# Kernel tuning notes

Measured on AMD Instinct MI355X. Metric: run time of the kernel, lower is better.

## Reference

```python
import jax, jax.numpy as jnp
import numpy as np

B, F0, D = 4096, 39, 16
CIN = [128, 128, 128]


def setup_inputs() -> dict:
    key = jax.random.key(0)
    ks = jax.random.split(key, 4)
    x = jax.random.normal(ks[0], (B, F0, D), dtype=jnp.float32)
    fields = [F0] + CIN
    inp = {"embedded_features": x}
    for i in range(len(CIN)):
        cin = F0 * fields[i]
        cout = fields[i + 1]
        kw = jax.random.fold_in(ks[1], i)
        # Conv1d default init scale ~ 1/sqrt(fan_in)
        inp[f"W{i}"] = jax.random.normal(kw, (cout, cin), dtype=jnp.float32) / np.sqrt(cin)
        inp[f"b{i}"] = jnp.zeros((cout,), dtype=jnp.float32)
    return inp


def _cin_layer(X0, Xi, W, b):
    # Math identical to: outer_product [B,F0,Fi,D] -> reshape [B,F0*Fi,D] -> 1x1 Conv1d.
    # Conv1d(kernel=1) over the flattened F0*Fi channel dim is a contraction over (j,k):
    #   Xn[b,h,d] = sum_{j,k} W[h, j*Fi+k] * X0[b,j,d] * Xi[b,k,d] + b[h]
    H = W.shape[0]
    F0_, Fi = X0.shape[1], Xi.shape[1]
    Wr = W.reshape(H, F0_, Fi)
    return jnp.einsum('hjk,bjd,bkd->bhd', Wr, X0, Xi) + b[None, :, None]


def reference(embedded_features, W0, b0, W1, b1, W2, b2):
    X0 = embedded_features  # [B, F0, D]
    Ws = [(W0, b0), (W1, b1), (W2, b2)]
    Xi = X0
    res = []
    for W, b in Ws:
        Xi = _cin_layer(X0, Xi, W, b)  # [B, H_i, D]
        res.append(Xi.sum(axis=2))     # sum over embedding dim
    return jnp.concatenate(res, axis=1)  # [B, sum(cin_size)]
```

## Files before the change

### kernel.cpp

```cpp
#include <hip/hip_runtime.h>
#include <stdint.h>


#define NB_F0 39
#define NB_H  128
#define NB_B  4096

typedef float f32x4  __attribute__((ext_vector_type(4)));
typedef float f32x16 __attribute__((ext_vector_type(16)));
typedef short s16x8  __attribute__((ext_vector_type(8)));

__device__ __forceinline__ void dma16(const void* g, void* l) {
  __builtin_amdgcn_global_load_lds(
      (const __attribute__((address_space(1))) unsigned int*)g,
      (__attribute__((address_space(3))) unsigned int*)l, 16, 0, 0);
}

__device__ __forceinline__ unsigned short rne_bf16(float f) {
  union { float f; unsigned u; } v; v.f = f;
  return (unsigned short)((v.u + 0x7fffu + ((v.u >> 16) & 1u)) >> 16);
}
__device__ __forceinline__ float bf16_to_f32(unsigned short s) {
  union { unsigned u; float f; } v; v.u = ((unsigned)s) << 16;
  return v.f;
}

__global__ void prep_x0_kernel(const float* __restrict__ X0g,
                               unsigned short* __restrict__ X0T,
                               unsigned short* __restrict__ X0c) {
  const int b = blockIdx.x;
  const int t = threadIdx.x;
  {
    const int d  = t >> 4;
    const int k4 = (t & 15) << 2;
    unsigned short vv[4];
#pragma unroll
    for (int i = 0; i < 4; ++i) {
      const int k = k4 + i;
      vv[i] = (k < NB_F0) ? rne_bf16(X0g[(size_t)b * (NB_F0 * 16) + k * 16 + d])
                          : (unsigned short)0;
    }
    ushort4 pk; pk.x = vv[0]; pk.y = vv[1]; pk.z = vv[2]; pk.w = vv[3];
    *(ushort4*)&X0T[((size_t)b * 16 + d) * 64 + k4] = pk;
  }
  for (int idx = t; idx < NB_F0 * 16; idx += 256) {
    const int j = idx >> 4, pos = idx & 15;
    const int d = (pos & 3) | (((pos >> 3) & 1) << 2) | (((pos >> 2) & 1) << 3);
    X0c[(size_t)b * (NB_F0 * 16) + idx] =
        rne_bf16(X0g[(size_t)b * (NB_F0 * 16) + j * 16 + d]);
  }
}

__global__ void prep_w_kernel(const float* __restrict__ Wsrc,
                              unsigned short* __restrict__ Wdst,
                              int Fi, int kshift, int total) {
  int idx = blockIdx.x * 256 + threadIdx.x;
  if (idx >= total) return;
  const int i    = idx & 7;
  const int lane = (idx >> 3) & 63;
  const int c    = (idx >> 9) & ((1 << kshift) - 1);
  const int jt   = idx >> (9 + kshift);
  const int t    = jt & 3;
  const int j    = jt >> 2;
  const int h = t * 32 + (lane & 31);
  const int k = c * 16 + ((lane >> 5) << 3) + i;
  unsigned short v = 0;
  if (k < Fi) v = rne_bf16(Wsrc[(size_t)h * (NB_F0 * Fi) + j * Fi + k]);
  Wdst[idx] = v;
}

template <int FI_PAD, bool STORE_XN>
__global__ __launch_bounds__(256, 4) void cin_layer(
    const unsigned short* __restrict__ Wf,
    const unsigned short* __restrict__ XiT,
    const unsigned short* __restrict__ X0c,
    const float* __restrict__ bias,
    unsigned short* __restrict__ XnT,
    float* __restrict__ outp)
{
  constexpr int KPASS = FI_PAD / 64;
  constexpr int KC16  = FI_PAD / 16;
  constexpr int S     = NB_F0 * KPASS;

  __shared__ __attribute__((aligned(16))) unsigned short Wlds[4][2048];
  __shared__ __attribute__((aligned(16))) unsigned short x0s[16 * NB_F0 * 16];

  const int tid  = threadIdx.x;
  const int lane = tid & 63;
  const int wv   = tid >> 6;
  const int L    = lane >> 5;
  const int col  = lane & 31;
  const int ht   = blockIdx.x >> 8;
  const int bblk = (blockIdx.x & 255) * 16;
  const int bwave = bblk + wv * 4;

  auto dma_stage = [&](int s, int buf) {
    const int pass = (KPASS == 2 && s >= NB_F0) ? 1 : 0;
    const int j = s - pass * NB_F0;
    const unsigned short* src =
        Wf + (((size_t)(j * 4 + ht) * KC16) + pass * 4 + wv) * 512 + lane * 8;
    dma16(src, &Wlds[buf][wv * 512]);
  };

  {
    const unsigned short* src = X0c + (size_t)bblk * (NB_F0 * 16);
    for (int c = tid; c < (16 * NB_F0 * 16) / 8; c += 256)
      *(s16x8*)&x0s[c * 8] = *(const s16x8*)&src[c * 8];
  }

  s16x8 af[2][4];
  auto load_af = [&](int pass) {
#pragma unroll
    for (int P = 0; P < 2; ++P) {
      const unsigned short* base = XiT +
          ((size_t)(bwave + 2 * P + (col >> 4)) * 16 + (col & 15)) * FI_PAD +
          pass * 64 + L * 8;
#pragma unroll
      for (int c = 0; c < 4; ++c) af[P][c] = *(const s16x8*)(base + c * 16);
    }
  };
  load_af(0);

  f32x16 Xacc[2], kZero;
#pragma unroll
  for (int r = 0; r < 16; ++r) kZero[r] = 0.f;
#pragma unroll
  for (int P = 0; P < 2; ++P) Xacc[P] = kZero;

  __syncthreads();

  dma_stage(0, 0);
  dma_stage(1, 1);
  dma_stage(2, 2);

  const int x0base = (wv * 4) * (NB_F0 * 16) + L * 8;

  auto body = [&](int s) {
    asm volatile("s_waitcnt vmcnt(2)" ::: "memory");
    __builtin_amdgcn_s_barrier();
    asm volatile("" ::: "memory");

    const int sn = s + 3;
    dma_stage(sn < S ? sn : sn - S, sn & 3);

    const int j = (KPASS == 2 && s >= NB_F0) ? s - NB_F0 : s;
    const unsigned short* wb = &Wlds[s & 3][lane * 8];
    const s16x8 w0 = *(const s16x8*)(wb);
    const s16x8 w1 = *(const s16x8*)(wb + 512);
    const s16x8 w2 = *(const s16x8*)(wb + 1024);
    const s16x8 w3 = *(const s16x8*)(wb + 1536);

#pragma unroll
    for (int P = 0; P < 2; ++P) {
      f32x16 y;
      y = __builtin_amdgcn_mfma_f32_32x32x16_bf16(af[P][0], w0, kZero, 0, 0, 0);
      y = __builtin_amdgcn_mfma_f32_32x32x16_bf16(af[P][1], w1, y, 0, 0, 0);
      y = __builtin_amdgcn_mfma_f32_32x32x16_bf16(af[P][2], w2, y, 0, 0, 0);
      y = __builtin_amdgcn_mfma_f32_32x32x16_bf16(af[P][3], w3, y, 0, 0, 0);

      const uint4 xu0 = *(const uint4*)
          &x0s[x0base + (2 * P + 0) * (NB_F0 * 16) + j * 16];
      const uint4 xu1 = *(const uint4*)
          &x0s[x0base + (2 * P + 1) * (NB_F0 * 16) + j * 16];
      const unsigned wd[8] = {xu0.x, xu0.y, xu0.z, xu0.w,
                              xu1.x, xu1.y, xu1.z, xu1.w};
      f32x16 xsc;
#pragma unroll
      for (int i = 0; i < 8; ++i) {
        xsc[2 * i]     = __uint_as_float(wd[i] << 16);
        xsc[2 * i + 1] = __uint_as_float(wd[i] & 0xffff0000u);
      }
      Xacc[P] = __builtin_elementwise_fma(xsc, y, Xacc[P]);
    }
  };

  int s = 0;
  for (; s < NB_F0; ++s) body(s);
  if (KPASS == 2) {
    load_af(1);
    for (; s < S; ++s) body(s);
  }

  const float bias_v = bias[ht * 32 + col];
#pragma unroll
  for (int P = 0; P < 2; ++P) {
#pragma unroll
    for (int bh = 0; bh < 2; ++bh) {
      const int b = bwave + 2 * P + bh;
      float v[8];
#pragma unroll
      for (int m = 0; m < 8; ++m) v[m] = Xacc[P][bh * 8 + m] + bias_v;
      if (STORE_XN) {
#pragma unroll
        for (int m = 0; m < 8; ++m) {
          const int d = (m & 3) + 8 * ((m >> 2) & 1) + 4 * L;
          XnT[((size_t)b * 16 + d) * NB_H + ht * 32 + col] = rne_bf16(v[m]);
        }
      }
      float tot = ((v[0] + v[1]) + (v[2] + v[3])) + ((v[4] + v[5]) + (v[6] + v[7]));
      tot += __shfl_xor(tot, 32);
      if (lane < 32) outp[(size_t)b * 384 + ht * 32 + lane] = tot;
    }
  }
}

extern "C" void kernel_launch(void* const* d_in, const int* in_sizes, int n_in,
                              void* d_out, int out_size, void* d_ws, size_t ws_size,
                              hipStream_t stream) {
  (void)in_sizes; (void)n_in; (void)out_size; (void)ws_size;
  const float* X0g = (const float*)d_in[0];
  const float* W0  = (const float*)d_in[1];
  const float* b0  = (const float*)d_in[2];
  const float* W1  = (const float*)d_in[3];
  const float* b1  = (const float*)d_in[4];
  const float* W2  = (const float*)d_in[5];
  const float* b2  = (const float*)d_in[6];
  float* out = (float*)d_out;

  char* p = (char*)d_ws;
  unsigned short* X0T = (unsigned short*)p; p += (size_t)NB_B * 16 * 64 * 2;
  unsigned short* X0c = (unsigned short*)p; p += (size_t)NB_B * NB_F0 * 16 * 2;
  unsigned short* X1T = (unsigned short*)p; p += (size_t)NB_B * 16 * 128 * 2;
  unsigned short* X2T = (unsigned short*)p; p += (size_t)NB_B * 16 * 128 * 2;
  unsigned short* Wf0 = (unsigned short*)p; p += (size_t)NB_F0 * 4 * 4 * 512 * 2;
  unsigned short* Wf1 = (unsigned short*)p; p += (size_t)NB_F0 * 4 * 8 * 512 * 2;
  unsigned short* Wf2 = (unsigned short*)p; p += (size_t)NB_F0 * 4 * 8 * 512 * 2;

  hipLaunchKernelGGL(prep_x0_kernel, dim3(NB_B), dim3(256), 0, stream,
                     X0g, X0T, X0c);
  const int tw0  = NB_F0 * 4 * 4 * 512;
  const int tw12 = NB_F0 * 4 * 8 * 512;
  hipLaunchKernelGGL(prep_w_kernel, dim3((tw0 + 255) / 256), dim3(256), 0, stream,
                     W0, Wf0, 39, 2, tw0);
  hipLaunchKernelGGL(prep_w_kernel, dim3((tw12 + 255) / 256), dim3(256), 0, stream,
                     W1, Wf1, 128, 3, tw12);
  hipLaunchKernelGGL(prep_w_kernel, dim3((tw12 + 255) / 256), dim3(256), 0, stream,
                     W2, Wf2, 128, 3, tw12);

  hipLaunchKernelGGL((cin_layer<64, true>),   dim3(1024), dim3(256), 0, stream,
                     Wf0, X0T, X0c, b0, X1T, out + 0);
  hipLaunchKernelGGL((cin_layer<128, true>),  dim3(1024), dim3(256), 0, stream,
                     Wf1, X1T, X0c, b1, X2T, out + 128);
  hipLaunchKernelGGL((cin_layer<128, false>), dim3(1024), dim3(256), 0, stream,
                     Wf2, X2T, X0c, b2, (unsigned short*)nullptr, out + 256);
}
```

Measured before the change: 311.8 us.

## Shrink CIN blocks to two waves and fuse both K passes into one loop

Each cin_layer block now covers 8 batch rows with 2 waves of 128 threads instead of 16 rows with 4 waves, so the launch grid doubles to 2048 blocks. Every stage now DMAs the full K extent of weights for field j into LDS, with a 3-buffer ring and a prefetch distance of 2. All of Xi stays in registers (KC16 chunks) and the second K pass over the fields is gone, so each field's X0 scaling is applied once per full-K MFMA chain. The aim is to halve the number of barrier-separated stages for Fi=128 and to cut redundant loop overhead. In exchange, register pressure rises and each block reuses the weights it loads across fewer batch rows.

Result: slower. 370.4 us (+18.8%).

```diff
diff --git a/kernel.cpp b/kernel.cpp
--- a/kernel.cpp
+++ b/kernel.cpp
@@ -70,7 +70,7 @@
 }
 
 template <int FI_PAD, bool STORE_XN>
-__global__ __launch_bounds__(256, 4) void cin_layer(
+__global__ __launch_bounds__(128, 2) void cin_layer(
     const unsigned short* __restrict__ Wf,
     const unsigned short* __restrict__ XiT,
     const unsigned short* __restrict__ X0c,
@@ -78,48 +78,47 @@
     unsigned short* __restrict__ XnT,
     float* __restrict__ outp)
 {
-  constexpr int KPASS = FI_PAD / 64;
-  constexpr int KC16  = FI_PAD / 16;
-  constexpr int S     = NB_F0 * KPASS;
-
-  __shared__ __attribute__((aligned(16))) unsigned short Wlds[4][2048];
-  __shared__ __attribute__((aligned(16))) unsigned short x0s[16 * NB_F0 * 16];
+  constexpr int KC16 = FI_PAD / 16;
+  constexpr int CPW  = KC16 / 2;
+  constexpr int S    = NB_F0;
+
+  __shared__ __attribute__((aligned(16))) unsigned short Wlds[3][KC16 * 512];
+  __shared__ __attribute__((aligned(16))) unsigned short x0s[8 * NB_F0 * 16];
 
   const int tid  = threadIdx.x;
   const int lane = tid & 63;
   const int wv   = tid >> 6;
   const int L    = lane >> 5;
   const int col  = lane & 31;
-  const int ht   = blockIdx.x >> 8;
-  const int bblk = (blockIdx.x & 255) * 16;
+  const int ht   = blockIdx.x >> 9;
+  const int bblk = (blockIdx.x & 511) * 8;
   const int bwave = bblk + wv * 4;
 
-  auto dma_stage = [&](int s, int buf) {
-    const int pass = (KPASS == 2 && s >= NB_F0) ? 1 : 0;
-    const int j = s - pass * NB_F0;
-    const unsigned short* src =
-        Wf + (((size_t)(j * 4 + ht) * KC16) + pass * 4 + wv) * 512 + lane * 8;
-    dma16(src, &Wlds[buf][wv * 512]);
+  auto dma_stage = [&](int j, int buf) {
+#pragma unroll
+    for (int cc = 0; cc < CPW; ++cc) {
+      const int c = CPW * wv + cc;
+      const unsigned short* src =
+          Wf + ((size_t)(j * 4 + ht) * KC16 + c) * 512 + lane * 8;
+      dma16(src, &Wlds[buf][c * 512]);
+    }
   };
 
   {
     const unsigned short* src = X0c + (size_t)bblk * (NB_F0 * 16);
-    for (int c = tid; c < (16 * NB_F0 * 16) / 8; c += 256)
+    for (int c = tid; c < (8 * NB_F0 * 16) / 8; c += 128)
       *(s16x8*)&x0s[c * 8] = *(const s16x8*)&src[c * 8];
   }
 
-  s16x8 af[2][4];
-  auto load_af = [&](int pass) {
-#pragma unroll
-    for (int P = 0; P < 2; ++P) {
-      const unsigned short* base = XiT +
-          ((size_t)(bwave + 2 * P + (col >> 4)) * 16 + (col & 15)) * FI_PAD +
-          pass * 64 + L * 8;
-#pragma unroll
-      for (int c = 0; c < 4; ++c) af[P][c] = *(const s16x8*)(base + c * 16);
-    }
-  };
-  load_af(0);
+  s16x8 af[2][KC16];
+#pragma unroll
+  for (int P = 0; P < 2; ++P) {
+    const unsigned short* base = XiT +
+        ((size_t)(bwave + 2 * P + (col >> 4)) * 16 + (col & 15)) * FI_PAD +
+        L * 8;
+#pragma unroll
+    for (int c = 0; c < KC16; ++c) af[P][c] = *(const s16x8*)(base + c * 16);
+  }
 
   f32x16 Xacc[2], kZero;
 #pragma unroll
@@ -131,37 +130,37 @@
 
   dma_stage(0, 0);
   dma_stage(1, 1);
-  dma_stage(2, 2);
 
   const int x0base = (wv * 4) * (NB_F0 * 16) + L * 8;
 
-  auto body = [&](int s) {
-    asm volatile("s_waitcnt vmcnt(2)" ::: "memory");
+  int bc = 0;
+  for (int s = 0; s < S; ++s) {
+    if constexpr (CPW == 4) asm volatile("s_waitcnt vmcnt(4)" ::: "memory");
+    else                    asm volatile("s_waitcnt vmcnt(2)" ::: "memory");
     __builtin_amdgcn_s_barrier();
     asm volatile("" ::: "memory");
 
-    const int sn = s + 3;
-    dma_stage(sn < S ? sn : sn - S, sn & 3);
-
-    const int j = (KPASS == 2 && s >= NB_F0) ? s - NB_F0 : s;
-    const unsigned short* wb = &Wlds[s & 3][lane * 8];
-    const s16x8 w0 = *(const s16x8*)(wb);
-    const s16x8 w1 = *(const s16x8*)(wb + 512);
-    const s16x8 w2 = *(const s16x8*)(wb + 1024);
-    const s16x8 w3 = *(const s16x8*)(wb + 1536);
+    const int bp = bc == 0 ? 2 : bc - 1;
+    const int sn = s + 2;
+    dma_stage(sn < S ? sn : sn - S, bp);
+
+    const unsigned short* wb = &Wlds[bc][lane * 8];
+    s16x8 w[KC16];
+#pragma unroll
+    for (int c = 0; c < KC16; ++c) w[c] = *(const s16x8*)(wb + c * 512);
 
 #pragma unroll
     for (int P = 0; P < 2; ++P) {
-      f32x16 y;
-      y = __builtin_amdgcn_mfma_f32_32x32x16_bf16(af[P][0], w0, kZero, 0, 0, 0);
-      y = __builtin_amdgcn_mfma_f32_32x32x16_bf16(af[P][1], w1, y, 0, 0, 0);
-      y = __builtin_amdgcn_mfma_f32_32x32x16_bf16(af[P][2], w2, y, 0, 0, 0);
-      y = __builtin_amdgcn_mfma_f32_32x32x16_bf16(af[P][3], w3, y, 0, 0, 0);
+      f32x16 y = __builtin_amdgcn_mfma_f32_32x32x16_bf16(af[P][0], w[0],
+                                                         kZero, 0, 0, 0);
+#pragma unroll
+      for (int c = 1; c < KC16; ++c)
+        y = __builtin_amdgcn_mfma_f32_32x32x16_bf16(af[P][c], w[c], y, 0, 0, 0);
 
       const uint4 xu0 = *(const uint4*)
-          &x0s[x0base + (2 * P + 0) * (NB_F0 * 16) + j * 16];
+          &x0s[x0base + (2 * P + 0) * (NB_F0 * 16) + s * 16];
       const uint4 xu1 = *(const uint4*)
-          &x0s[x0base + (2 * P + 1) * (NB_F0 * 16) + j * 16];
+          &x0s[x0base + (2 * P + 1) * (NB_F0 * 16) + s * 16];
       const unsigned wd[8] = {xu0.x, xu0.y, xu0.z, xu0.w,
                               xu1.x, xu1.y, xu1.z, xu1.w};
       f32x16 xsc;
@@ -172,13 +171,8 @@
       }
       Xacc[P] = __builtin_elementwise_fma(xsc, y, Xacc[P]);
     }
-  };
-
-  int s = 0;
-  for (; s < NB_F0; ++s) body(s);
-  if (KPASS == 2) {
-    load_af(1);
-    for (; s < S; ++s) body(s);
+
+    bc = bc == 2 ? 0 : bc + 1;
   }
 
   const float bias_v = bias[ht * 32 + col];
@@ -237,10 +231,10 @@
   hipLaunchKernelGGL(prep_w_kernel, dim3((tw12 + 255) / 256), dim3(256), 0, stream,
                      W2, Wf2, 128, 3, tw12);
 
-  hipLaunchKernelGGL((cin_layer<64, true>),   dim3(1024), dim3(256), 0, stream,
+  hipLaunchKernelGGL((cin_layer<64, true>),   dim3(2048), dim3(128), 0, stream,
                      Wf0, X0T, X0c, b0, X1T, out + 0);
-  hipLaunchKernelGGL((cin_layer<128, true>),  dim3(1024), dim3(256), 0, stream,
+  hipLaunchKernelGGL((cin_layer<128, true>),  dim3(2048), dim3(128), 0, stream,
                      Wf1, X1T, X0c, b1, X2T, out + 128);
-  hipLaunchKernelGGL((cin_layer<128, false>), dim3(1024), dim3(256), 0, stream,
+  hipLaunchKernelGGL((cin_layer<128, false>), dim3(2048), dim3(128), 0, stream,
                      Wf2, X2T, X0c, b2, (unsigned short*)nullptr, out + 256);
 }
```
